# Kernel tuning notes

Hardware: AMD Instinct MI355X
Metric: run time of the kernel (lower is better)

Reference implementation:

```python
import jax, jax.numpy as jnp
import numpy as np

B, C, H, W = 4, 8, 384, 384
NUM_LAYERS = 5
CG_ITERS = 10


def conv2d(x, w, b):
    # x: [B,Cin,H,W], w: [Cout,Cin,3,3]
    y = jax.lax.conv_general_dilated(x, w, (1, 1), 'SAME',
                                     dimension_numbers=('NCHW', 'OIHW', 'NCHW'))
    return y + b[None, :, None, None]


def dw(x, w_in, b_in, ws_mid, bs_mid, w_out, b_out):
    # Sequence: conv, conv, relu, conv, conv, relu, conv, conv, relu, conv, conv, relu, conv
    h = conv2d(x, w_in, b_in)
    for i in range(7):
        h = conv2d(h, ws_mid[i], bs_mid[i])
        if i % 2 == 0:  # ReLU after convs 2,4,6,8
            h = jax.nn.relu(h)
    h = conv2d(h, w_out, b_out)
    return x + h  # residual


def conjugate_grad(rhs, csm_c, mask, lam):
    # rhs: [B,H,W] complex; csm_c: [B,C,H,W] complex; mask: [B,H,W] real
    def AtA(p):
        coil = csm_c * p[:, None]                      # [B,C,H,W]
        k = jnp.fft.fft2(coil) * mask[:, None]         # masked k-space
        return jnp.sum(jnp.conj(csm_c) * jnp.fft.ifft2(k), axis=1)

    def body(carry, _):
        x, r, p, rTr = carry
        Ap = AtA(p) + lam * p
        pAp = jnp.sum(jnp.conj(p) * Ap, axis=(-2, -1)).real
        alpha = rTr / pAp
        x = x + alpha[:, None, None] * p
        r = r - alpha[:, None, None] * Ap
        rTrNew = jnp.sum(jnp.conj(r) * r, axis=(-2, -1)).real
        beta = rTrNew / rTr
        p = r + beta[:, None, None] * p
        return (x, r, p, rTrNew), None

    x0 = jnp.zeros_like(rhs)
    rTr0 = jnp.sum(jnp.conj(rhs) * rhs, axis=(-2, -1)).real
    (x, _, _, _), _ = jax.lax.scan(body, (x0, rhs, rhs, rTr0), None, length=CG_ITERS)
    return x


def reference(under_img, csm, mask, lam, w_in, b_in, ws_mid, bs_mid, w_out, b_out):
    csm_c = jax.lax.complex(csm[..., 0], csm[..., 1])  # [B,C,H,W] complex
    lam_s = lam[0]
    x = under_img
    for _ in range(NUM_LAYERS):
        x = dw(x, w_in, b_in, ws_mid, bs_mid, w_out, b_out)
        x = under_img + lam_s * x
        rhs = jax.lax.complex(x[:, 0], x[:, 1])        # view_as_complex(permute(0,2,3,1))
        xc = conjugate_grad(rhs, csm_c, mask, lam_s)
        x = jnp.stack([xc.real, xc.imag], axis=1)      # view_as_real -> [B,2,H,W]
    return x


def setup_inputs() -> dict:
    key = jax.random.key(0)
    ks = jax.random.split(key, 8)
    under_img = jax.random.normal(ks[0], (B, 2, H, W), jnp.float32)
    csm = jax.random.normal(ks[1], (B, C, H, W, 2), jnp.float32) / np.sqrt(C)
    mask = (jax.random.uniform(ks[2], (B, H, W)) > 0.5).astype(jnp.float32)
    lam = jnp.array([0.05], jnp.float32)
    w_in = jax.random.normal(ks[3], (64, 2, 3, 3), jnp.float32) * 0.02
    b_in = jnp.zeros((64,), jnp.float32)
    ws_mid = jax.random.normal(ks[4], (7, 64, 64, 3, 3), jnp.float32) * 0.02
    bs_mid = jnp.zeros((7, 64), jnp.float32)
    w_out = jax.random.normal(ks[5], (2, 64, 3, 3), jnp.float32) * 0.02
    b_out = jnp.zeros((2,), jnp.float32)
    return {"under_img": under_img, "csm": csm, "mask": mask, "lam": lam,
            "w_in": w_in, "b_in": b_in, "ws_mid": ws_mid, "bs_mid": bs_mid,
            "w_out": w_out, "b_out": b_out}
```

## Files before the change

kernel.cpp:

```cpp
#include <hip/hip_runtime.h>
#include <hip/hip_bf16.h>
#include <hip/hip_fp16.h>
#include <math.h>

#define HH 384
#define WW 384
#define HW (HH*WW)
#define WP 386
#define PP (386*386)
#define BB 4
#define CC 8
#define NLAYERS 5
#define CGITERS 10
#define PI_F 3.14159265358979323846f

typedef __attribute__((ext_vector_type(8))) short short8;
typedef __attribute__((ext_vector_type(4))) float floatx4;

struct cf { float x, y; };
__device__ __forceinline__ cf cadd(cf a, cf b){ cf r; r.x=a.x+b.x; r.y=a.y+b.y; return r; }
__device__ __forceinline__ cf csub(cf a, cf b){ cf r; r.x=a.x-b.x; r.y=a.y-b.y; return r; }
__device__ __forceinline__ cf cmul(cf a, cf b){ cf r; r.x=a.x*b.x - a.y*b.y; r.y=a.x*b.y + a.y*b.x; return r; }
__device__ __forceinline__ cf csqr(cf a){ cf r; r.x = a.x*a.x - a.y*a.y; r.y = 2.f*a.x*a.y; return r; }
__device__ __forceinline__ cf shflxor(cf v, int m){ cf r; r.x = __shfl_xor(v.x, m); r.y = __shfl_xor(v.y, m); return r; }
__device__ __forceinline__ int brev7(int l){ return (int)(__brev((unsigned)l) >> 25); }
__device__ __forceinline__ int padi(int i){ return i + (i >> 3); }

__device__ __forceinline__ unsigned packh(cf v) {
  __half hx = __float2half(fminf(fmaxf(v.x, -60000.f), 60000.f));
  __half hy = __float2half(fminf(fmaxf(v.y, -60000.f), 60000.f));
  unsigned short ux = *(unsigned short*)&hx, uy = *(unsigned short*)&hy;
  return (unsigned)ux | ((unsigned)uy << 16);
}
__device__ __forceinline__ cf unpackh(unsigned u) {
  unsigned short ux = (unsigned short)(u & 0xffffu), uy = (unsigned short)(u >> 16);
  __half hx = *(__half*)&ux, hy = *(__half*)&uy;
  cf r; r.x = __half2float(hx); r.y = __half2float(hy); return r;
}

__device__ __forceinline__ void radix3(cf a0, cf a1, cf a2, float s3, cf y[3]) {
  float tx = a1.x + a2.x, ty_ = a1.y + a2.y;
  float ux = a1.x - a2.x, uy = a1.y - a2.y;
  y[0].x = a0.x + tx;              y[0].y = a0.y + ty_;
  y[1].x = a0.x - 0.5f*tx - s3*uy; y[1].y = a0.y - 0.5f*ty_ + s3*ux;
  y[2].x = a0.x - 0.5f*tx + s3*uy; y[2].y = a0.y - 0.5f*ty_ - s3*ux;
}

template<int SIGN>
__device__ __forceinline__ void fft384_wave(int l, const cf v[6], cf uA[3], cf uB[3]) {
  const float s3 = SIGN * 0.8660254037844386f;
  radix3(v[0], v[2], v[4], s3, uA);
  radix3(v[1], v[3], v[5], s3, uB);
  float sA, cA;
  __sincosf(SIGN * (2.0f * PI_F / 384.0f) * (float)l, &sA, &cA);
  cf wA1; wA1.x = cA; wA1.y = sA;
  cf wA2 = csqr(wA1);
  cf w6; w6.x = 0.5f; w6.y = s3;
  cf wB1 = cmul(wA1, w6);
  cf wB2 = csqr(wB1);
  uA[1] = cmul(uA[1], wA1); uA[2] = cmul(uA[2], wA2);
  uB[1] = cmul(uB[1], wB1); uB[2] = cmul(uB[2], wB2);
  cf u = cmul(wA2, wA1);
  #pragma unroll
  for (int k1 = 0; k1 < 3; ++k1) {
    cf a = uA[k1], b = uB[k1];
    uA[k1] = cadd(a, b);
    uB[k1] = cmul(csub(a, b), u);
  }
  #pragma unroll
  for (int h = 32; h >= 1; h >>= 1) {
    u = csqr(u);
    const bool up = (l & h) != 0;
    #pragma unroll
    for (int k1 = 0; k1 < 3; ++k1) {
      cf pa = shflxor(uA[k1], h);
      cf pb = shflxor(uB[k1], h);
      cf na = up ? cmul(csub(uA[k1], pa), u) : cadd(uA[k1], pa);
      cf nb = up ? cmul(csub(uB[k1], pb), u) : cadd(uB[k1], pb);
      uA[k1] = na; uB[k1] = nb;
    }
  }
}


__global__ void repack_mid_k(const float* __restrict__ ws_mid, __hip_bfloat16* __restrict__ wrep) {
  const int idx = blockIdx.x * 256 + threadIdx.x;
  if (idx >= 7*9*64*64) return;
  const int ci = idx & 63, co = (idx >> 6) & 63, tap = (idx >> 12) % 9, i = idx / (9*4096);
  wrep[idx] = __float2bfloat16(ws_mid[(((size_t)i*64 + co)*64 + ci)*9 + tap]);
}

__global__ void zero_guard_k(__hip_bfloat16* __restrict__ a, __hip_bfloat16* __restrict__ b2) {
  const int idx = blockIdx.x * 256 + threadIdx.x;
  if (idx >= 2*BB*1540*8) return;
  const int s = idx & 7; int rest = idx >> 3;
  const int px = rest % 1540; rest /= 1540;
  const int bb = rest & 3; const int buf = rest >> 2;
  int row, col;
  if (px < WP)        { row = 0;    col = px; }
  else if (px < 2*WP) { row = HH+1; col = px - WP; }
  else { const int k = px - 2*WP; row = 1 + (k >> 1); col = (k & 1) ? (WW+1) : 0; }
  __hip_bfloat16* base = buf ? b2 : a;
  *(uint4*)(base + ((size_t)bb*PP + (size_t)row*WP + col)*64 + s*8) = make_uint4(0u,0u,0u,0u);
}

__global__ void __launch_bounds__(256) conv_in_k(const float* __restrict__ xin,
                                                 const float* __restrict__ w,
                                                 const float* __restrict__ bias,
                                                 __hip_bfloat16* __restrict__ out) {
  __shared__ float tile[2][340];
  const int tx = threadIdx.x & 31, ty = threadIdx.x >> 5;
  const int x0 = blockIdx.x * 32, y0 = blockIdx.y * 8, b = blockIdx.z;
  for (int e = threadIdx.x; e < 680; e += 256) {
    int ci = e / 340, rr = e % 340;
    int iy = y0 - 1 + rr / 34, ix = x0 - 1 + rr % 34;
    float v = 0.f;
    if (iy >= 0 && iy < HH && ix >= 0 && ix < WW)
      v = xin[(b*2 + ci)*HW + iy*WW + ix];
    tile[ci][rr] = v;
  }
  __syncthreads();
  float acc[64];
  #pragma unroll
  for (int co = 0; co < 64; ++co) acc[co] = bias[co];
  #pragma unroll
  for (int ci = 0; ci < 2; ++ci) {
    float v0 = tile[ci][ty*34+tx],     v1 = tile[ci][ty*34+tx+1],     v2 = tile[ci][ty*34+tx+2];
    float v3 = tile[ci][(ty+1)*34+tx], v4 = tile[ci][(ty+1)*34+tx+1], v5 = tile[ci][(ty+1)*34+tx+2];
    float v6 = tile[ci][(ty+2)*34+tx], v7 = tile[ci][(ty+2)*34+tx+1], v8 = tile[ci][(ty+2)*34+tx+2];
    #pragma unroll
    for (int co = 0; co < 64; ++co) {
      const float* wp = w + co*18 + ci*9;
      float a = acc[co];
      a = fmaf(v0, wp[0], a); a = fmaf(v1, wp[1], a); a = fmaf(v2, wp[2], a);
      a = fmaf(v3, wp[3], a); a = fmaf(v4, wp[4], a); a = fmaf(v5, wp[5], a);
      a = fmaf(v6, wp[6], a); a = fmaf(v7, wp[7], a); a = fmaf(v8, wp[8], a);
      acc[co] = a;
    }
  }
  const size_t obase = ((size_t)b*PP + (size_t)(y0 + ty + 1)*WP + (x0 + tx + 1))*64;
  #pragma unroll
  for (int s = 0; s < 8; ++s) {
    uint4 u;
    __hip_bfloat16* hp = (__hip_bfloat16*)&u;
    #pragma unroll
    for (int j = 0; j < 8; ++j) hp[j] = __float2bfloat16(acc[s*8 + j]);
    *(uint4*)(out + obase + s*8) = u;
  }
}

__global__ void __launch_bounds__(256) conv_mid_mfma_k(
    const __hip_bfloat16* __restrict__ in,
    const __hip_bfloat16* __restrict__ wrep,
    const float* __restrict__ bias,
    __hip_bfloat16* __restrict__ out, int relu) {
  __shared__ __align__(16) __hip_bfloat16 atile[2752*8];
  const int tid = threadIdx.x;
  const int l = tid & 63, wv = tid >> 6;
  const int x0 = blockIdx.x * 32, y0 = blockIdx.y * 8, b = blockIdx.z;

  const int kseg = l >> 4;
  const int lr = l & 15;

  const __hip_bfloat16* wlane = wrep + lr*64 + kseg*8;
  short8 bf[4][2];
  #pragma unroll
  for (int nt = 0; nt < 4; ++nt) {
    bf[nt][0] = *(const short8*)(wlane + nt*1024);
    bf[nt][1] = *(const short8*)(wlane + nt*1024 + 32);
  }

  const __hip_bfloat16* inb = in + (size_t)b*PP*64;
  #pragma unroll
  for (int i = 0; i < 10; ++i) {
    const int j = i*256 + tid;
    const int p = j >> 3, s = j & 7;
    const int g = s ^ (p & 7);
    const __hip_bfloat16* src = inb + ((size_t)(y0 + p/34)*WP + (x0 + p%34))*64 + g*8;
    __builtin_amdgcn_global_load_lds(
        (const __attribute__((address_space(1))) void*)src,
        (__attribute__((address_space(3))) void*)(atile + (i*256 + wv*64)*8),
        16, 0, 0);
  }
  if (tid < 160) {
    const int j = 2560 + tid;
    const int p = j >> 3, s = j & 7;
    const int g = s ^ (p & 7);
    uint4 v = *(const uint4*)(inb + ((size_t)(y0 + p/34)*WP + (x0 + p%34))*64 + g*8);
    *(uint4*)(atile + j*8) = v;
  }

  floatx4 acc[4][4];
  #pragma unroll
  for (int mt = 0; mt < 4; ++mt)
    #pragma unroll
    for (int nt = 0; nt < 4; ++nt)
      acc[mt][nt] = (floatx4){0.f, 0.f, 0.f, 0.f};

  __syncthreads();

  #pragma unroll 1
  for (int tap = 0; tap < 9; ++tap) {
    short8 bfn[4][2];
    if (tap < 8) {
      const __hip_bfloat16* wn = wlane + (tap + 1)*4096;
      #pragma unroll
      for (int nt = 0; nt < 4; ++nt) {
        bfn[nt][0] = *(const short8*)(wn + nt*1024);
        bfn[nt][1] = *(const short8*)(wn + nt*1024 + 32);
      }
    }
    const int dy = tap / 3, dx = tap - dy*3;
    short8 af[4][2];
    #pragma unroll
    for (int mt = 0; mt < 4; ++mt) {
      const int ry = 2*wv + (mt >> 1) + dy;
      const int px = (mt & 1)*16 + lr + dx;
      const int p  = ry*34 + px;
      const int eo = p*64 + ((kseg ^ (p & 7)) << 3);
      af[mt][0] = *(const short8*)(atile + eo);
      af[mt][1] = *(const short8*)(atile + (eo ^ 32));
    }
    #pragma unroll
    for (int mt = 0; mt < 4; ++mt)
      #pragma unroll
      for (int nt = 0; nt < 4; ++nt) {
        acc[mt][nt] = __builtin_amdgcn_mfma_f32_16x16x32_bf16(af[mt][0], bf[nt][0], acc[mt][nt], 0, 0, 0);
        acc[mt][nt] = __builtin_amdgcn_mfma_f32_16x16x32_bf16(af[mt][1], bf[nt][1], acc[mt][nt], 0, 0, 0);
      }
    if (tap < 8) {
      #pragma unroll
      for (int nt = 0; nt < 4; ++nt) { bf[nt][0] = bfn[nt][0]; bf[nt][1] = bfn[nt][1]; }
    }
  }

  __syncthreads();
  __hip_bfloat16* otile = atile;
  #pragma unroll
  for (int mt = 0; mt < 4; ++mt) {
    const int row = 2*wv + (mt >> 1);
    #pragma unroll
    for (int nt = 0; nt < 4; ++nt) {
      const int ch = nt*16 + lr;
      const float bv = bias[ch];
      #pragma unroll
      for (int rr = 0; rr < 4; ++rr) {
        const int px = (mt & 1)*16 + kseg*4 + rr;
        float v = acc[mt][nt][rr] + bv;
        if (relu) v = fmaxf(v, 0.f);
        otile[(row*32 + px)*72 + ch] = __float2bfloat16(v);
      }
    }
  }
  __syncthreads();
  #pragma unroll
  for (int iter = 0; iter < 8; ++iter) {
    const int p = iter*32 + (tid >> 3), s = tid & 7;
    const int row = p >> 5, px = p & 31;
    uint4 v = *(const uint4*)(&otile[p*72 + s*8]);
    *(uint4*)(out + ((size_t)b*PP + (size_t)(y0 + row + 1)*WP + (x0 + px + 1))*64 + s*8) = v;
  }
}

__global__ void __launch_bounds__(256) conv_out_k(const __hip_bfloat16* __restrict__ in,
                                                  const float* __restrict__ w,
                                                  const float* __restrict__ bias,
                                                  const float* __restrict__ xcur,
                                                  const float* __restrict__ under,
                                                  const float* __restrict__ lam,
                                                  cf* __restrict__ r, cf* __restrict__ p,
                                                  cf* __restrict__ xc, float* __restrict__ scL) {
  __shared__ __hip_bfloat16 atile[340*72];
  __shared__ float wl[2*64*9];
  __shared__ float wsum[4];
  const int tid = threadIdx.x;
  const int tx = tid & 31, ty = tid >> 5;
  const int x0 = blockIdx.x * 32, y0 = blockIdx.y * 8, b = blockIdx.z;

  for (int e = tid; e < 340*8; e += 256) {
    int pp = e >> 3, s = e & 7;
    uint4 v = *(const uint4*)(in + ((size_t)b*PP + (size_t)(y0 + pp/34)*WP + (x0 + pp%34))*64 + s*8);
    *(uint4*)(&atile[pp*72 + s*8]) = v;
  }
  for (int e = tid; e < 2*64*9; e += 256) wl[e] = w[e];
  __syncthreads();

  float a0 = bias[0], a1 = bias[1];
  #pragma unroll 1
  for (int tap = 0; tap < 9; ++tap) {
    const int dy = tap / 3, dx = tap - dy*3;
    const __hip_bfloat16* ap = &atile[((ty + dy)*34 + tx + dx)*72];
    #pragma unroll
    for (int s = 0; s < 8; ++s) {
      short8 v8 = *(const short8*)(ap + s*8);
      const __hip_bfloat16* hv = (const __hip_bfloat16*)&v8;
      #pragma unroll
      for (int j = 0; j < 8; ++j) {
        const float f = __bfloat162float(hv[j]);
        a0 = fmaf(f, wl[(s*8 + j)*9 + tap], a0);
        a1 = fmaf(f, wl[(64 + s*8 + j)*9 + tap], a1);
      }
    }
  }
  const float lamv = lam[0];
  const int y = y0 + ty, x = x0 + tx;
  const int idx2 = y*WW + x;
  float xv0 = xcur[b*2*HW + idx2],  xv1 = xcur[b*2*HW + HW + idx2];
  float u0  = under[b*2*HW + idx2], u1  = under[b*2*HW + HW + idx2];
  float r0 = u0 + lamv * (xv0 + a0);
  float r1 = u1 + lamv * (xv1 + a1);
  const int cidx = b*HW + idx2;
  cf vv; vv.x = r0; vv.y = r1;
  r[cidx] = vv; p[cidx] = vv;
  cf zz; zz.x = 0.f; zz.y = 0.f; xc[cidx] = zz;
  float partial = r0*r0 + r1*r1;
  for (int off = 32; off; off >>= 1) partial += __shfl_down(partial, off);
  const int l = tid & 63, wvid = tid >> 6;
  if (l == 0) wsum[wvid] = partial;
  __syncthreads();
  if (tid == 0) atomicAdd(&scL[b], wsum[0]+wsum[1]+wsum[2]+wsum[3]);
}


__global__ void __launch_bounds__(256) update_k(const cf* __restrict__ rold, cf* __restrict__ rnew,
                                                const cf* __restrict__ pold, cf* __restrict__ pnew,
                                                cf* __restrict__ xc, const cf* __restrict__ Ap,
                                                float* __restrict__ scL, int it) {
  const int idx = blockIdx.x * 256 + threadIdx.x;
  const int b = idx / HW;
  const float rtrp  = scL[(it-1)*4 + b];
  const float pApp  = scL[40 + (it-1)*4 + b];
  const float ApApp = scL[80 + (it-1)*4 + b];
  const float alpha = rtrp / pApp;
  const float rtrn  = alpha*alpha*ApApp - rtrp;
  const float beta  = rtrn / rtrp;
  if ((idx - b*HW) == 0) scL[it*4 + b] = rtrn;
  cf rv = rold[idx];
  cf av = Ap[idx];
  rv.x -= alpha*av.x; rv.y -= alpha*av.y;
  cf po = pold[idx];
  cf pv; pv.x = rv.x + beta*po.x; pv.y = rv.y + beta*po.y;
  rnew[idx] = rv;
  pnew[idx] = pv;
  cf xv = xc[idx]; xv.x += alpha*po.x; xv.y += alpha*po.y; xc[idx] = xv;
}

__global__ void __launch_bounds__(256) pass_a_k(const cf* __restrict__ pin,
                                                const cf* __restrict__ csm,
                                                unsigned* __restrict__ t) {
  __shared__ cf rowbuf[4][434];
  const int l = threadIdx.x & 63, wv = threadIdx.x >> 6;
  const int y = blockIdx.x * 4 + wv;
  const int c = blockIdx.y, b = blockIdx.z;
  const cf* prow = pin + b*HW + y*WW;
  const cf* crow = csm + (b*CC + c)*HW + y*WW;
  cf v[6];
  #pragma unroll
  for (int m = 0; m < 6; ++m) v[m] = cmul(crow[l + 64*m], prow[l + 64*m]);
  cf uA[3], uB[3];
  fft384_wave<-1>(l, v, uA, uB);
  const int R3 = 3 * brev7(l);
  cf* rb = rowbuf[wv];
  #pragma unroll
  for (int k1 = 0; k1 < 3; ++k1) { rb[padi(k1 + R3)] = uA[k1]; rb[padi(k1 + R3 + 3)] = uB[k1]; }
  unsigned* trow = t + (b*CC + c)*HW + y*WW;
  #pragma unroll
  for (int m = 0; m < 6; ++m) trow[l + 64*m] = packh(rb[padi(l + 64*m)]);
}

__global__ void __launch_bounds__(256) pass_b_k(unsigned* __restrict__ t, const float* __restrict__ mask) {
  __shared__ cf tile[431*9];
  const int b = blockIdx.z, c = blockIdx.y, x0 = blockIdx.x * 8;
  unsigned* base = t + (b*CC + c)*HW;
  for (int e = threadIdx.x; e < 3072; e += 256) {
    int y = e >> 3, xx = e & 7;
    tile[padi(y)*9 + xx] = unpackh(base[y*WW + x0 + xx]);
  }
  __syncthreads();
  const int l = threadIdx.x & 63, wv = threadIdx.x >> 6;
  const int R3 = 3 * brev7(l);
  for (int rep = 0; rep < 2; ++rep) {
    const int xx = wv*2 + rep, x = x0 + xx;
    cf v[6];
    #pragma unroll
    for (int m = 0; m < 6; ++m) v[m] = tile[padi(l + 64*m)*9 + xx];
    cf uA[3], uB[3];
    fft384_wave<-1>(l, v, uA, uB);
    const float* mrow = mask + b*HW + x;
    #pragma unroll
    for (int k1 = 0; k1 < 3; ++k1) {
      float mA = mrow[(k1 + R3)*WW], mB = mrow[(k1 + R3 + 3)*WW];
      uA[k1].x *= mA; uA[k1].y *= mA; uB[k1].x *= mB; uB[k1].y *= mB;
    }
    __syncthreads();
    #pragma unroll
    for (int k1 = 0; k1 < 3; ++k1) { tile[padi(k1 + R3)*9 + xx] = uA[k1]; tile[padi(k1 + R3 + 3)*9 + xx] = uB[k1]; }
    __syncthreads();
    #pragma unroll
    for (int m = 0; m < 6; ++m) v[m] = tile[padi(l + 64*m)*9 + xx];
    fft384_wave<1>(l, v, uA, uB);
    const float s = 1.0f / 384.0f;
    #pragma unroll
    for (int k1 = 0; k1 < 3; ++k1) {
      uA[k1].x *= s; uA[k1].y *= s; uB[k1].x *= s; uB[k1].y *= s;
      tile[padi(k1 + R3)*9 + xx] = uA[k1]; tile[padi(k1 + R3 + 3)*9 + xx] = uB[k1];
    }
    __syncthreads();
  }
  for (int e = threadIdx.x; e < 3072; e += 256) {
    int y = e >> 3, xx = e & 7;
    base[y*WW + x0 + xx] = packh(tile[padi(y)*9 + xx]);
  }
}

__global__ void __launch_bounds__(256) pass_c_k(const unsigned* __restrict__ t, const cf* __restrict__ csm,
                                                const cf* __restrict__ p, cf* __restrict__ Ap,
                                                const float* __restrict__ lam,
                                                float* __restrict__ scL, int it) {
  __shared__ cf rowbuf[4][2][434];
  __shared__ cf redbuf[4][384];
  __shared__ float wsums[4][2];
  const int tid = threadIdx.x;
  const int l = tid & 63, wv = tid >> 6;
  const int y = blockIdx.x, b = blockIdx.y;
  const int R3 = 3 * brev7(l);
  cf acc[6] = {};
  #pragma unroll
  for (int ci = 0; ci < 2; ++ci) {
    const int c = wv*2 + ci;
    const unsigned* trow = t + (b*CC + c)*HW + y*WW;
    cf v[6];
    #pragma unroll
    for (int m = 0; m < 6; ++m) v[m] = unpackh(trow[l + 64*m]);
    cf uA[3], uB[3];
    fft384_wave<1>(l, v, uA, uB);
    cf* rb = rowbuf[wv][ci];
    #pragma unroll
    for (int k1 = 0; k1 < 3; ++k1) { rb[padi(k1 + R3)] = uA[k1]; rb[padi(k1 + R3 + 3)] = uB[k1]; }
    const cf* crow = csm + (b*CC + c)*HW + y*WW;
    #pragma unroll
    for (int m = 0; m < 6; ++m) {
      cf cs = crow[l + 64*m];
      cf wz = rb[padi(l + 64*m)];
      acc[m].x += cs.x*wz.x + cs.y*wz.y;
      acc[m].y += cs.x*wz.y - cs.y*wz.x;
    }
  }
  #pragma unroll
  for (int m = 0; m < 6; ++m) redbuf[wv][m*64 + l] = acc[m];
  __syncthreads();

  const float lamv = lam[0];
  const float sc384 = 1.0f / 384.0f;
  const cf* prow = p + b*HW + y*WW;
  cf* aprow = Ap + b*HW + y*WW;
  float partial = 0.f, partial2 = 0.f;
  #pragma unroll
  for (int rep = 0; rep < 2; ++rep) {
    const int pos = rep*256 + tid;
    if (pos < 384) {
      cf s0 = redbuf[0][pos], s1 = redbuf[1][pos], s2 = redbuf[2][pos], s3 = redbuf[3][pos];
      cf s; s.x = (s0.x + s1.x) + (s2.x + s3.x); s.y = (s0.y + s1.y) + (s2.y + s3.y);
      cf pv = prow[pos];
      cf ap; ap.x = s.x*sc384 + lamv*pv.x; ap.y = s.y*sc384 + lamv*pv.y;
      aprow[pos] = ap;
      partial  += pv.x*ap.x + pv.y*ap.y;
      partial2 += ap.x*ap.x + ap.y*ap.y;
    }
  }
  #pragma unroll
  for (int off = 32; off; off >>= 1) {
    partial  += __shfl_down(partial, off);
    partial2 += __shfl_down(partial2, off);
  }
  if (l == 0) { wsums[wv][0] = partial; wsums[wv][1] = partial2; }
  __syncthreads();
  if (tid == 0) {
    atomicAdd(&scL[40 + it*4 + b], (wsums[0][0]+wsums[1][0])+(wsums[2][0]+wsums[3][0]));
    atomicAdd(&scL[80 + it*4 + b], (wsums[0][1]+wsums[1][1])+(wsums[2][1]+wsums[3][1]));
  }
}

__global__ void __launch_bounds__(256) final_x_k(const cf* __restrict__ xc, const cf* __restrict__ p9,
                                                 const float* __restrict__ scL, float* __restrict__ out) {
  const int idx = blockIdx.x * 256 + threadIdx.x;
  const int b = idx / HW;
  const int rem = idx - b*HW;
  const float alpha = scL[(CGITERS-1)*4 + b] / scL[40 + (CGITERS-1)*4 + b];
  cf xv = xc[idx], pv = p9[idx];
  xv.x += alpha*pv.x; xv.y += alpha*pv.y;
  out[b*2*HW + rem] = xv.x;
  out[b*2*HW + HW + rem] = xv.y;
}

__global__ void zero_sc_k(float* sc) {
  for (int i = threadIdx.x; i < NLAYERS*128; i += 256) sc[i] = 0.f;
}

extern "C" void kernel_launch(void* const* d_in, const int* in_sizes, int n_in,
                              void* d_out, int out_size, void* d_ws, size_t ws_size,
                              hipStream_t stream) {
  (void)in_sizes; (void)n_in; (void)out_size; (void)ws_size;
  const float* under  = (const float*)d_in[0];
  const cf*    csm    = (const cf*)d_in[1];
  const float* mask   = (const float*)d_in[2];
  const float* lam    = (const float*)d_in[3];
  const float* w_in   = (const float*)d_in[4];
  const float* b_in   = (const float*)d_in[5];
  const float* ws_mid = (const float*)d_in[6];
  const float* bs_mid = (const float*)d_in[7];
  const float* w_out  = (const float*)d_in[8];
  const float* b_out  = (const float*)d_in[9];
  float* xcur = (float*)d_out;

  char* bws = (char*)d_ws;
  size_t off = 0;
  auto carve = [&](size_t bytes) { char* pp = bws + off; off += (bytes + 255) & ~(size_t)255; return (void*)pp; };
  __hip_bfloat16* actA = (__hip_bfloat16*)carve((size_t)BB*PP*64*2);
  __hip_bfloat16* actB = (__hip_bfloat16*)carve((size_t)BB*PP*64*2);
  unsigned* t = (unsigned*)carve((size_t)BB*CC*HW*4);
  cf* rbuf0 = (cf*)carve((size_t)BB*HW*8);
  cf* rbuf1 = (cf*)carve((size_t)BB*HW*8);
  cf* pbuf0 = (cf*)carve((size_t)BB*HW*8);
  cf* pbuf1 = (cf*)carve((size_t)BB*HW*8);
  cf* xc    = (cf*)carve((size_t)BB*HW*8);
  cf* Ap    = (cf*)carve((size_t)BB*HW*8);
  float* sc = (float*)carve(4096);
  __hip_bfloat16* wrep = (__hip_bfloat16*)carve((size_t)7*9*64*64*2);

  hipMemcpyAsync(xcur, under, (size_t)BB*2*HW*sizeof(float), hipMemcpyDeviceToDevice, stream);

  zero_sc_k<<<1, 256, 0, stream>>>(sc);
  repack_mid_k<<<(7*9*64*64 + 255)/256, 256, 0, stream>>>(ws_mid, wrep);
  zero_guard_k<<<(2*BB*1540*8 + 255)/256, 256, 0, stream>>>(actA, actB);

  dim3 cgrid(WW/32, HH/8, BB);
  dim3 agrid(HH/4, CC, BB);
  dim3 bgrid(WW/8, CC, BB);
  dim3 c2grid(HH, BB);
  const int egrid = BB*HW/256;

  __hip_bfloat16* bufs[2] = { actA, actB };
  cf* rb[2] = { rbuf0, rbuf1 };
  cf* pb[2] = { pbuf0, pbuf1 };

  for (int layer = 0; layer < NLAYERS; ++layer) {
    float* scL = sc + layer*128;
    conv_in_k<<<cgrid, 256, 0, stream>>>(xcur, w_in, b_in, bufs[0]);
    for (int i = 0; i < 7; ++i) {
      conv_mid_mfma_k<<<cgrid, 256, 0, stream>>>(bufs[i & 1], wrep + (size_t)i*9*4096,
                                                 bs_mid + i*64, bufs[(i + 1) & 1], (i % 2 == 0) ? 1 : 0);
    }
    conv_out_k<<<cgrid, 256, 0, stream>>>(bufs[1], w_out, b_out, xcur, under, lam,
                                          rbuf0, pbuf0, xc, scL);
    for (int it = 0; it < CGITERS; ++it) {
      cf* rold = rb[(it + 1) & 1];
      cf* rnew = rb[it & 1];
      cf* pold = pb[(it + 1) & 1];
      cf* pnew = pb[it & 1];
      if (it == 0) { rold = rbuf0; pold = pbuf0; rnew = rbuf0; pnew = pbuf0; }
      if (it > 0)
        update_k<<<egrid, 256, 0, stream>>>(rold, rnew, pold, pnew, xc, Ap, scL, it);
      pass_a_k<<<agrid, 256, 0, stream>>>(pnew, csm, t);
      pass_b_k<<<bgrid, 256, 0, stream>>>(t, mask);
      pass_c_k<<<c2grid, 256, 0, stream>>>(t, csm, pnew, Ap, lam, scL, it);
    }
    final_x_k<<<egrid, 256, 0, stream>>>(xc, pb[(CGITERS - 1) & 1], scL, xcur);
  }
}
```

Before: 8.978 ms.

## Fuse CG update into row-FFT pass and store coil maps in half precision

The separate CG vector update kernel is folded into the first FFT pass. Each wave now updates one row of r, p and x and then loops over all 8 coils, reusing the updated p row from registers, so one launch and a re-read of p per coil are removed. Coil sensitivity maps are packed once into half-precision complex words, which halves their bandwidth in passes A and C but lowers the precision of csm. Blocks shrink to 128 threads, giving a smaller grid with more serial work per wave.

Measured after the change: 9.453 ms. +5.3%, slower.

```diff
diff --git a/kernel.cpp b/kernel.cpp
--- a/kernel.cpp
+++ b/kernel.cpp
@@ -90,6 +90,12 @@
   wrep[idx] = __float2bfloat16(ws_mid[(((size_t)i*64 + co)*64 + ci)*9 + tap]);
 }
 
+__global__ void repack_csm_k(const cf* __restrict__ csm, unsigned* __restrict__ csmh) {
+  const int idx = blockIdx.x * 256 + threadIdx.x;
+  if (idx >= BB*CC*HW) return;
+  csmh[idx] = packh(csm[idx]);
+}
+
 __global__ void zero_guard_k(__hip_bfloat16* __restrict__ a, __hip_bfloat16* __restrict__ b2) {
   const int idx = blockIdx.x * 256 + threadIdx.x;
   if (idx >= 2*BB*1540*8) return;
@@ -321,51 +327,58 @@
   if (tid == 0) atomicAdd(&scL[b], wsum[0]+wsum[1]+wsum[2]+wsum[3]);
 }
 
-
-__global__ void __launch_bounds__(256) update_k(const cf* __restrict__ rold, cf* __restrict__ rnew,
+__global__ void __launch_bounds__(128) pass_a_k(const cf* __restrict__ rold, cf* __restrict__ rnew,
                                                 const cf* __restrict__ pold, cf* __restrict__ pnew,
                                                 cf* __restrict__ xc, const cf* __restrict__ Ap,
+                                                const unsigned* __restrict__ csmh,
+                                                unsigned* __restrict__ t,
                                                 float* __restrict__ scL, int it) {
-  const int idx = blockIdx.x * 256 + threadIdx.x;
-  const int b = idx / HW;
-  const float rtrp  = scL[(it-1)*4 + b];
-  const float pApp  = scL[40 + (it-1)*4 + b];
-  const float ApApp = scL[80 + (it-1)*4 + b];
-  const float alpha = rtrp / pApp;
-  const float rtrn  = alpha*alpha*ApApp - rtrp;
-  const float beta  = rtrn / rtrp;
-  if ((idx - b*HW) == 0) scL[it*4 + b] = rtrn;
-  cf rv = rold[idx];
-  cf av = Ap[idx];
-  rv.x -= alpha*av.x; rv.y -= alpha*av.y;
-  cf po = pold[idx];
-  cf pv; pv.x = rv.x + beta*po.x; pv.y = rv.y + beta*po.y;
-  rnew[idx] = rv;
-  pnew[idx] = pv;
-  cf xv = xc[idx]; xv.x += alpha*po.x; xv.y += alpha*po.y; xc[idx] = xv;
-}
-
-__global__ void __launch_bounds__(256) pass_a_k(const cf* __restrict__ pin,
-                                                const cf* __restrict__ csm,
-                                                unsigned* __restrict__ t) {
-  __shared__ cf rowbuf[4][434];
+  __shared__ cf rowbuf[2][434];
   const int l = threadIdx.x & 63, wv = threadIdx.x >> 6;
-  const int y = blockIdx.x * 4 + wv;
-  const int c = blockIdx.y, b = blockIdx.z;
-  const cf* prow = pin + b*HW + y*WW;
-  const cf* crow = csm + (b*CC + c)*HW + y*WW;
-  cf v[6];
-  #pragma unroll
-  for (int m = 0; m < 6; ++m) v[m] = cmul(crow[l + 64*m], prow[l + 64*m]);
-  cf uA[3], uB[3];
-  fft384_wave<-1>(l, v, uA, uB);
+  const int y = blockIdx.x * 2 + wv;
+  const int b = blockIdx.y;
+  const int rowoff = b*HW + y*WW;
+  cf pv[6];
+  if (it == 0) {
+    #pragma unroll
+    for (int m = 0; m < 6; ++m) pv[m] = pold[rowoff + l + 64*m];
+  } else {
+    const float rtrp  = scL[(it-1)*4 + b];
+    const float pApp  = scL[40 + (it-1)*4 + b];
+    const float ApApp = scL[80 + (it-1)*4 + b];
+    const float alpha = rtrp / pApp;
+    const float rtrn  = alpha*alpha*ApApp - rtrp;
+    const float beta  = rtrn / rtrp;
+    if (blockIdx.x == 0 && threadIdx.x == 0) scL[it*4 + b] = rtrn;
+    #pragma unroll
+    for (int m = 0; m < 6; ++m) {
+      const int idx = rowoff + l + 64*m;
+      cf rv = rold[idx];
+      cf av = Ap[idx];
+      rv.x -= alpha*av.x; rv.y -= alpha*av.y;
+      cf po = pold[idx];
+      pv[m].x = rv.x + beta*po.x; pv[m].y = rv.y + beta*po.y;
+      rnew[idx] = rv;
+      pnew[idx] = pv[m];
+      cf xv = xc[idx]; xv.x += alpha*po.x; xv.y += alpha*po.y; xc[idx] = xv;
+    }
+  }
   const int R3 = 3 * brev7(l);
   cf* rb = rowbuf[wv];
-  #pragma unroll
-  for (int k1 = 0; k1 < 3; ++k1) { rb[padi(k1 + R3)] = uA[k1]; rb[padi(k1 + R3 + 3)] = uB[k1]; }
-  unsigned* trow = t + (b*CC + c)*HW + y*WW;
-  #pragma unroll
-  for (int m = 0; m < 6; ++m) trow[l + 64*m] = packh(rb[padi(l + 64*m)]);
+  #pragma unroll 1
+  for (int c = 0; c < CC; ++c) {
+    const unsigned* crow = csmh + (b*CC + c)*HW + y*WW;
+    cf v[6];
+    #pragma unroll
+    for (int m = 0; m < 6; ++m) v[m] = cmul(unpackh(crow[l + 64*m]), pv[m]);
+    cf uA[3], uB[3];
+    fft384_wave<-1>(l, v, uA, uB);
+    #pragma unroll
+    for (int k1 = 0; k1 < 3; ++k1) { rb[padi(k1 + R3)] = uA[k1]; rb[padi(k1 + R3 + 3)] = uB[k1]; }
+    unsigned* trow = t + (b*CC + c)*HW + y*WW;
+    #pragma unroll
+    for (int m = 0; m < 6; ++m) trow[l + 64*m] = packh(rb[padi(l + 64*m)]);
+  }
 }
 
 __global__ void __launch_bounds__(256) pass_b_k(unsigned* __restrict__ t, const float* __restrict__ mask) {
@@ -413,7 +426,8 @@
   }
 }
 
-__global__ void __launch_bounds__(256) pass_c_k(const unsigned* __restrict__ t, const cf* __restrict__ csm,
+__global__ void __launch_bounds__(256) pass_c_k(const unsigned* __restrict__ t,
+                                                const unsigned* __restrict__ csmh,
                                                 const cf* __restrict__ p, cf* __restrict__ Ap,
                                                 const float* __restrict__ lam,
                                                 float* __restrict__ scL, int it) {
@@ -437,10 +451,10 @@
     cf* rb = rowbuf[wv][ci];
     #pragma unroll
     for (int k1 = 0; k1 < 3; ++k1) { rb[padi(k1 + R3)] = uA[k1]; rb[padi(k1 + R3 + 3)] = uB[k1]; }
-    const cf* crow = csm + (b*CC + c)*HW + y*WW;
+    const unsigned* crow = csmh + (b*CC + c)*HW + y*WW;
     #pragma unroll
     for (int m = 0; m < 6; ++m) {
-      cf cs = crow[l + 64*m];
+      cf cs = unpackh(crow[l + 64*m]);
       cf wz = rb[padi(l + 64*m)];
       acc[m].x += cs.x*wz.x + cs.y*wz.y;
       acc[m].y += cs.x*wz.y - cs.y*wz.x;
@@ -518,7 +532,8 @@
   auto carve = [&](size_t bytes) { char* pp = bws + off; off += (bytes + 255) & ~(size_t)255; return (void*)pp; };
   __hip_bfloat16* actA = (__hip_bfloat16*)carve((size_t)BB*PP*64*2);
   __hip_bfloat16* actB = (__hip_bfloat16*)carve((size_t)BB*PP*64*2);
-  unsigned* t = (unsigned*)carve((size_t)BB*CC*HW*4);
+  unsigned* t    = (unsigned*)carve((size_t)BB*CC*HW*4);
+  unsigned* csmh = (unsigned*)carve((size_t)BB*CC*HW*4);
   cf* rbuf0 = (cf*)carve((size_t)BB*HW*8);
   cf* rbuf1 = (cf*)carve((size_t)BB*HW*8);
   cf* pbuf0 = (cf*)carve((size_t)BB*HW*8);
@@ -532,10 +547,11 @@
 
   zero_sc_k<<<1, 256, 0, stream>>>(sc);
   repack_mid_k<<<(7*9*64*64 + 255)/256, 256, 0, stream>>>(ws_mid, wrep);
+  repack_csm_k<<<(BB*CC*HW + 255)/256, 256, 0, stream>>>(csm, csmh);
   zero_guard_k<<<(2*BB*1540*8 + 255)/256, 256, 0, stream>>>(actA, actB);
 
   dim3 cgrid(WW/32, HH/8, BB);
-  dim3 agrid(HH/4, CC, BB);
+  dim3 agrid(HH/2, BB);
   dim3 bgrid(WW/8, CC, BB);
   dim3 c2grid(HH, BB);
   const int egrid = BB*HW/256;
@@ -559,11 +575,9 @@
       cf* pold = pb[(it + 1) & 1];
       cf* pnew = pb[it & 1];
       if (it == 0) { rold = rbuf0; pold = pbuf0; rnew = rbuf0; pnew = pbuf0; }
-      if (it > 0)
-        update_k<<<egrid, 256, 0, stream>>>(rold, rnew, pold, pnew, xc, Ap, scL, it);
-      pass_a_k<<<agrid, 256, 0, stream>>>(pnew, csm, t);
+      pass_a_k<<<agrid, 128, 0, stream>>>(rold, rnew, pold, pnew, xc, Ap, csmh, t, scL, it);
       pass_b_k<<<bgrid, 256, 0, stream>>>(t, mask);
-      pass_c_k<<<c2grid, 256, 0, stream>>>(t, csm, pnew, Ap, lam, scL, it);
+      pass_c_k<<<c2grid, 256, 0, stream>>>(t, csmh, pnew, Ap, lam, scL, it);
     }
     final_x_k<<<egrid, 256, 0, stream>>>(xc, pb[(CGITERS - 1) & 1], scL, xcur);
   }
```
